# Kernel tuning notes

Hardware: AMD Instinct MI355X
Metric: run time of the kernel (lower is better)

## Reference

```python
import jax, jax.numpy as jnp
import numpy as np

N_NODES = 100000
N_EDGES = 1600000
D = 128
N_GRAPHS = 128
N_LAYERS = 3


def setup_inputs() -> dict:
    key = jax.random.key(0)
    ks = jax.random.split(key, 3 + 4 * N_LAYERS)
    x = jax.random.normal(ks[0], (N_NODES, D), dtype=jnp.float32)
    edge_index = jax.random.randint(ks[1], (2, N_EDGES), 0, N_NODES, dtype=jnp.int64)
    batch = jnp.sort(jax.random.randint(ks[2], (N_NODES,), 0, N_GRAPHS, dtype=jnp.int64))
    inp = {"x": x, "edge_index": edge_index, "batch": batch}
    scale = 1.0 / np.sqrt(D)
    for l in range(N_LAYERS):
        inp[f"W1_{l}"] = jax.random.normal(ks[3 + 4 * l], (D, D), dtype=jnp.float32) * scale
        inp[f"b1_{l}"] = jnp.zeros((D,), dtype=jnp.float32)
        inp[f"W2_{l}"] = jax.random.normal(ks[4 + 4 * l], (D, D), dtype=jnp.float32) * scale
        inp[f"b2_{l}"] = jnp.zeros((D,), dtype=jnp.float32)
    return inp


def _gin_conv(x, edge_index, W1, b1, W2, b2):
    # GINConv with eps=0: out = MLP(x + sum_{j in N(i)} x_j)
    msgs = x[edge_index[0]]                                   # [E, D] gather
    agg = jax.ops.segment_sum(msgs, edge_index[1], num_segments=N_NODES)
    h = x + agg
    h = jax.nn.relu(h @ W1 + b1)
    return h @ W2 + b2


def reference(x, edge_index, batch,
              W1_0, b1_0, W2_0, b2_0,
              W1_1, b1_1, W2_1, b2_1,
              W1_2, b1_2, W2_2, b2_2):
    params = [(W1_0, b1_0, W2_0, b2_0), (W1_1, b1_1, W2_1, b2_1), (W1_2, b1_2, W2_2, b2_2)]
    h = x
    for l in range(N_LAYERS - 1):
        h = _gin_conv(h, edge_index, *params[l])
        h = jax.nn.relu(h)  # act; dropout with drop_ratio=0 is identity
    node_emb = _gin_conv(h, edge_index, *params[-1])  # JK='last'
    # global_mean_pool
    sums = jax.ops.segment_sum(node_emb, batch, num_segments=N_GRAPHS)
    counts = jax.ops.segment_sum(jnp.ones((N_NODES, 1), node_emb.dtype), batch, num_segments=N_GRAPHS)
    graph_emb = sums / jnp.maximum(counts, 1.0)
    return graph_emb
```

## Files before the change

kernel.cpp:

```cpp
#include <hip/hip_runtime.h>
#include <hip/hip_bf16.h>

#define N_NODES 100000
#define N_PAD   100032
#define N_EDGES 1600000
#define DIM 128
#define N_GRAPHS 128
#define NBKT 98
#define BSTRIDE 18432
#define GRID_FUSED 3126
#define POOL_BLKS ((N_NODES + 127) / 128)
#define B1_BATCH 4096
#define B1_GRID ((N_EDGES + B1_BATCH - 1) / B1_BATCH)
#define XPREP_BLKS 12500
#define WPREP_BLKS 384
#define SUMS_BLKS 64

typedef unsigned short u16;
typedef unsigned int u32;
typedef __attribute__((ext_vector_type(8))) short bf16x8;
typedef __attribute__((ext_vector_type(8))) unsigned short u16x8;
typedef __attribute__((ext_vector_type(4))) float f32x4;

#define MFMA(A, B, C) __builtin_amdgcn_mfma_f32_16x16x32_bf16(A, B, C, 0, 0, 0)

__device__ __forceinline__ u16 f2bf(float x) {
    u32 u = __float_as_uint(x);
    u = (u + 0x7FFFu + ((u >> 16) & 1u)) >> 16;
    return (u16)u;
}
__device__ __forceinline__ float bf2f(u16 u) {
    return __uint_as_float(((u32)u) << 16);
}

__global__ __launch_bounds__(256) void bucket1_kernel(const int* __restrict__ src,
                                                      const int* __restrict__ dst,
                                                      u32* __restrict__ cursorB,
                                                      u32* __restrict__ pairs) {
    __shared__ int lh[NBKT];
    __shared__ u32 lbase[NBKT];
    int t = threadIdx.x;
    if (t < NBKT) lh[t] = 0;
    __syncthreads();
    int e0 = blockIdx.x * B1_BATCH;
    int d[16], s[16], rk[16];
#pragma unroll
    for (int k = 0; k < 16; ++k) {
        int e = e0 + t + k * 256;
        if (e < N_EDGES) {
            d[k] = dst[e];
            s[k] = src[e];
            rk[k] = atomicAdd(&lh[d[k] >> 10], 1);
        }
    }
    __syncthreads();
    if (t < NBKT) lbase[t] = atomicAdd(&cursorB[t], (u32)lh[t]) + (u32)(t * BSTRIDE);
    __syncthreads();
#pragma unroll
    for (int k = 0; k < 16; ++k) {
        int e = e0 + t + k * 256;
        if (e < N_EDGES) {
            u32 pos = lbase[d[k] >> 10] + (u32)rk[k];
            pairs[pos] = ((u32)(d[k] & 1023) << 22) | (u32)s[k];
        }
    }
}

__global__ __launch_bounds__(1024) void bucket2_kernel(const u32* __restrict__ cursorB,
                                                       const u32* __restrict__ pairs,
                                                       int* __restrict__ row_ptr,
                                                       int* __restrict__ csr) {
    __shared__ int lh[1024];
    __shared__ int rc[1024];
    __shared__ int bs[128];
    int b = blockIdx.x, t = threadIdx.x;

    if (t < 128) bs[t] = (t < NBKT) ? (int)cursorB[t] : 0;
    __syncthreads();
    for (int off = 1; off < 128; off <<= 1) {
        int v = (t < 128 && t >= off) ? bs[t - off] : 0;
        __syncthreads();
        if (t < 128) bs[t] += v;
        __syncthreads();
    }
    int cnt = (int)cursorB[b];
    int bbase = (b == 0) ? 0 : bs[b - 1];

    lh[t] = 0;
    __syncthreads();
    const u32* pb = pairs + (size_t)b * BSTRIDE;
    for (int i = t; i < cnt; i += 1024) atomicAdd(&lh[__builtin_nontemporal_load(pb + i) >> 22], 1);
    __syncthreads();

    int own = lh[t];
    for (int off = 1; off < 1024; off <<= 1) {
        int v = (t >= off) ? lh[t - off] : 0;
        __syncthreads();
        lh[t] += v;
        __syncthreads();
    }
    int excl = lh[t] - own;
    int node = b * 1024 + t;
    if (node < N_NODES) row_ptr[node] = bbase + excl;
    if (b == 0 && t == 0) row_ptr[N_NODES] = N_EDGES;
    rc[t] = bbase + excl;
    __syncthreads();

    for (int i = t; i < cnt; i += 1024) {
        u32 p = __builtin_nontemporal_load(pb + i);
        int pos = atomicAdd(&rc[p >> 22], 1);
        csr[pos] = (int)(p & 0x3FFFFFu);
    }
}

struct WPrepArgs {
    const float* w[6];
    u16* buf[6];
};
__global__ __launch_bounds__(256) void prep_kernel(const float* __restrict__ x,
                                                   u16* __restrict__ hb,
                                                   WPrepArgs p,
                                                   float* __restrict__ sums) {
    int b = blockIdx.x, t = threadIdx.x;
    if (b < XPREP_BLKS) {
        int i = b * 256 + t;
        if (i < N_NODES * 32) {
            float4 v = ((const float4*)x)[i];
            ushort4 o;
            o.x = f2bf(v.x); o.y = f2bf(v.y); o.z = f2bf(v.z); o.w = f2bf(v.w);
            ((ushort4*)hb)[i] = o;
        }
    } else if (b < XPREP_BLKS + WPREP_BLKS) {
        int bb = b - XPREP_BLKS;
        int m = bb >> 6;
        int idx = (bb & 63) * 256 + t;
        int n = idx >> 7, k = idx & 127;
        float v = p.w[m][k * 128 + n];
        u16 hi = f2bf(v);
        p.buf[m][idx] = hi;
        p.buf[m][idx + 16384] = f2bf(v - bf2f(hi));
    } else {
        int i = (b - XPREP_BLKS - WPREP_BLKS) * 256 + t;
        if (i < N_GRAPHS * DIM) sums[i] = 0.f;
    }
}

#define HS 136
__global__ __launch_bounds__(256, 4) void gin_layer(const u16* __restrict__ hin,
                                                    const int* __restrict__ rp,
                                                    const int* __restrict__ csr,
                                                    const u16* __restrict__ W1,
                                                    const float* __restrict__ b1,
                                                    const u16* __restrict__ W2,
                                                    const float* __restrict__ b2,
                                                    u16* __restrict__ hout, int relu) {
    __shared__ u16 Hh[32 * HS];
    __shared__ u16 Hl[32 * HS];
    int tid = threadIdx.x;
    int lane = tid & 63, wave = tid >> 6;
    int m16 = lane & 15, quad = lane >> 4;
    int colBase = wave * 32;
    int r0 = blockIdx.x * 32;

    {
        int qw = tid >> 4;
        int f  = tid & 15;
        const u16x8* h8 = (const u16x8*)hin;
#pragma unroll
        for (int j = 0; j < 2; ++j) {
            int nl = qw * 2 + j;
            int n = r0 + nl;
            float a[8];
            if (n < N_NODES) {
                u16x8 sv = h8[(size_t)n * 16 + f];
#pragma unroll
                for (int r = 0; r < 8; ++r) a[r] = bf2f(sv[r]);
                int s = rp[n], e = rp[n + 1];
                int i = s;
                for (; i + 8 <= e; i += 8) {
                    u16x8 v0 = h8[(size_t)csr[i + 0] * 16 + f];
                    u16x8 v1 = h8[(size_t)csr[i + 1] * 16 + f];
                    u16x8 v2 = h8[(size_t)csr[i + 2] * 16 + f];
                    u16x8 v3 = h8[(size_t)csr[i + 3] * 16 + f];
                    u16x8 v4 = h8[(size_t)csr[i + 4] * 16 + f];
                    u16x8 v5 = h8[(size_t)csr[i + 5] * 16 + f];
                    u16x8 v6 = h8[(size_t)csr[i + 6] * 16 + f];
                    u16x8 v7 = h8[(size_t)csr[i + 7] * 16 + f];
#pragma unroll
                    for (int r = 0; r < 8; ++r)
                        a[r] += ((bf2f(v0[r]) + bf2f(v1[r])) + (bf2f(v2[r]) + bf2f(v3[r]))) +
                                ((bf2f(v4[r]) + bf2f(v5[r])) + (bf2f(v6[r]) + bf2f(v7[r])));
                }
                for (; i < e; ++i) {
                    u16x8 v = h8[(size_t)csr[i] * 16 + f];
#pragma unroll
                    for (int r = 0; r < 8; ++r) a[r] += bf2f(v[r]);
                }
            } else {
#pragma unroll
                for (int r = 0; r < 8; ++r) a[r] = 0.f;
            }
            u16x8 o;
#pragma unroll
            for (int r = 0; r < 8; ++r) o[r] = f2bf(a[r]);
            *(u16x8*)&Hh[nl * HS + f * 8] = o;
        }
    }
    __syncthreads();

    bf16x8 aH[2][4];
#pragma unroll
    for (int p = 0; p < 2; ++p)
#pragma unroll
        for (int kb = 0; kb < 4; ++kb)
            aH[p][kb] = *(const bf16x8*)&Hh[(p * 16 + m16) * HS + kb * 32 + quad * 8];
    __syncthreads();

    float b1v[2][4], b2v[2][4];
#pragma unroll
    for (int nt = 0; nt < 2; ++nt)
#pragma unroll
        for (int rg = 0; rg < 4; ++rg) {
            int col = colBase + nt * 16 + quad * 4 + rg;
            b1v[nt][rg] = b1[col];
            b2v[nt][rg] = b2[col];
        }

    f32x4 z = {0.f, 0.f, 0.f, 0.f};

    bf16x8 W1H[2][4], W1L[2][4];
#pragma unroll
    for (int nt = 0; nt < 2; ++nt) {
        int n = colBase + nt * 16 + m16;
#pragma unroll
        for (int kb = 0; kb < 4; ++kb) {
            int off = n * 128 + kb * 32 + quad * 8;
            W1H[nt][kb] = *(const bf16x8*)(W1 + off);
            W1L[nt][kb] = *(const bf16x8*)(W1 + off + 16384);
        }
    }

    f32x4 acc[2][2];
#pragma unroll
    for (int p = 0; p < 2; ++p) { acc[p][0] = z; acc[p][1] = z; }

#pragma unroll
    for (int kb = 0; kb < 4; ++kb) {
#pragma unroll
        for (int p = 0; p < 2; ++p) {
            acc[p][0] = MFMA(W1H[0][kb], aH[p][kb], acc[p][0]);
            acc[p][1] = MFMA(W1H[1][kb], aH[p][kb], acc[p][1]);
            acc[p][0] = MFMA(W1L[0][kb], aH[p][kb], acc[p][0]);
            acc[p][1] = MFMA(W1L[1][kb], aH[p][kb], acc[p][1]);
        }
    }

#pragma unroll
    for (int p = 0; p < 2; ++p) {
#pragma unroll
        for (int nt = 0; nt < 2; ++nt) {
            ushort4 hv, lv;
#pragma unroll
            for (int rg = 0; rg < 4; ++rg) {
                float v = fmaxf(acc[p][nt][rg] + b1v[nt][rg], 0.f);
                u16 hi = f2bf(v);
                ((u16*)&hv)[rg] = hi;
                ((u16*)&lv)[rg] = f2bf(v - bf2f(hi));
            }
            int off = (p * 16 + m16) * HS + colBase + nt * 16 + quad * 4;
            *(ushort4*)&Hh[off] = hv;
            *(ushort4*)&Hl[off] = lv;
        }
    }
    __syncthreads();

    bf16x8 W2H[2][4], W2L[2][4];
#pragma unroll
    for (int nt = 0; nt < 2; ++nt) {
        int n = colBase + nt * 16 + m16;
#pragma unroll
        for (int kb = 0; kb < 4; ++kb) {
            int off = n * 128 + kb * 32 + quad * 8;
            W2H[nt][kb] = *(const bf16x8*)(W2 + off);
            W2L[nt][kb] = *(const bf16x8*)(W2 + off + 16384);
        }
    }

    f32x4 acc2[2][2];
#pragma unroll
    for (int p = 0; p < 2; ++p) { acc2[p][0] = z; acc2[p][1] = z; }
#pragma unroll
    for (int kb = 0; kb < 4; ++kb) {
#pragma unroll
        for (int p = 0; p < 2; ++p) {
            int off = (p * 16 + m16) * HS + kb * 32 + quad * 8;
            bf16x8 hH = *(const bf16x8*)(&Hh[off]);
            bf16x8 hL = *(const bf16x8*)(&Hl[off]);
            acc2[p][0] = MFMA(W2H[0][kb], hH, acc2[p][0]);
            acc2[p][1] = MFMA(W2H[1][kb], hH, acc2[p][1]);
            acc2[p][0] = MFMA(W2H[0][kb], hL, acc2[p][0]);
            acc2[p][1] = MFMA(W2H[1][kb], hL, acc2[p][1]);
            acc2[p][0] = MFMA(W2L[0][kb], hH, acc2[p][0]);
            acc2[p][1] = MFMA(W2L[1][kb], hH, acc2[p][1]);
        }
    }

#pragma unroll
    for (int p = 0; p < 2; ++p) {
        size_t row = (size_t)r0 + p * 16 + m16;
#pragma unroll
        for (int nt = 0; nt < 2; ++nt) {
            int col = colBase + nt * 16 + quad * 4;
            ushort4 o;
#pragma unroll
            for (int rg = 0; rg < 4; ++rg) {
                float v = acc2[p][nt][rg] + b2v[nt][rg];
                if (relu) v = fmaxf(v, 0.f);
                ((u16*)&o)[rg] = f2bf(v);
            }
            *(ushort4*)(hout + row * 128 + col) = o;
        }
    }
}

__global__ __launch_bounds__(256) void psum_kernel(const u16* __restrict__ h,
                                                   const int* __restrict__ batch,
                                                   float* __restrict__ sums) {
    __shared__ int sBatch[128];
    int blk = blockIdx.x, t = threadIdx.x;
    int n0 = blk * 128;
    int nEnd = min(n0 + 128, N_NODES);
    if (t < 128 && n0 + t < N_NODES) sBatch[t] = batch[n0 + t];
    __syncthreads();

    int j = t & 127;
    int half = t >> 7;
    int s = n0 + half * 64;
    int e = min(s + 64, nEnd);

    float acc = 0.f;
    int cur = -1;
    for (int n = s; n < e; ++n) {
        int g = sBatch[n - n0];
        if (g != cur) {
            if (cur >= 0) atomicAdd(&sums[cur * 128 + j], acc);
            cur = g;
            acc = 0.f;
        }
        acc += bf2f(h[(size_t)n * 128 + j]);
    }
    if (cur >= 0) atomicAdd(&sums[cur * 128 + j], acc);
}

__global__ __launch_bounds__(128) void pdiv_kernel(const float* __restrict__ sums,
                                                   const int* __restrict__ batch,
                                                   float* __restrict__ out) {
    __shared__ int sB[2];
    int g = blockIdx.x;
    if (threadIdx.x < 2) {
        int target = g + threadIdx.x;
        int lo = 0, hi = N_NODES;
        while (lo < hi) {
            int m = (lo + hi) >> 1;
            if (batch[m] < target) lo = m + 1; else hi = m;
        }
        sB[threadIdx.x] = lo;
    }
    __syncthreads();
    float cnt = (float)(sB[1] - sB[0]);
    out[g * 128 + threadIdx.x] = sums[g * 128 + threadIdx.x] / fmaxf(cnt, 1.f);
}

extern "C" void kernel_launch(void* const* d_in, const int* in_sizes, int n_in,
                              void* d_out, int out_size, void* d_ws, size_t ws_size,
                              hipStream_t stream) {
    const float* x     = (const float*)d_in[0];
    const int*   ei    = (const int*)d_in[1];
    const int*   batch = (const int*)d_in[2];
    const int*   eSrc  = ei;
    const int*   eDst  = ei + N_EDGES;

    const float* W1[3] = {(const float*)d_in[3], (const float*)d_in[7],  (const float*)d_in[11]};
    const float* b1[3] = {(const float*)d_in[4], (const float*)d_in[8],  (const float*)d_in[12]};
    const float* W2[3] = {(const float*)d_in[5], (const float*)d_in[9],  (const float*)d_in[13]};
    const float* b2[3] = {(const float*)d_in[6], (const float*)d_in[10], (const float*)d_in[14]};

    float* P2 = (float*)d_ws;
    u16*   planeB = (u16*)P2;
    u16*   planeA = (u16*)(P2 + (size_t)N_PAD * DIM);
    u16*   Ah = planeA + (size_t)N_PAD * DIM;
    u16*   Wb = Ah + (size_t)N_PAD * DIM;
    int*   row_ptr = (int*)(Wb + 6 * 32768);
    u32*   cursorB = (u32*)(row_ptr + N_NODES + 8);
    int*   csr     = (int*)(cursorB + 128);
    float* sums    = (float*)(csr + N_EDGES);
    u32*   pairs   = (u32*)P2;

    hipMemsetAsync(cursorB, 0, 128 * sizeof(u32), stream);
    bucket1_kernel<<<B1_GRID, 256, 0, stream>>>(eSrc, eDst, cursorB, pairs);
    bucket2_kernel<<<NBKT, 1024, 0, stream>>>(cursorB, pairs, row_ptr, csr);

    WPrepArgs wp;
    for (int l = 0; l < 3; ++l) {
        wp.w[2 * l]       = W1[l];
        wp.w[2 * l + 1]   = W2[l];
        wp.buf[2 * l]     = Wb + (size_t)(2 * l) * 32768;
        wp.buf[2 * l + 1] = Wb + (size_t)(2 * l + 1) * 32768;
    }
    prep_kernel<<<XPREP_BLKS + WPREP_BLKS + SUMS_BLKS, 256, 0, stream>>>(x, planeA, wp, sums);

    u16* hin  = planeA;
    u16* hout = planeB;
    for (int l = 0; l < 3; ++l) {
        gin_layer<<<GRID_FUSED, 256, 0, stream>>>(hin, row_ptr, csr,
                                                  Wb + (size_t)(2 * l) * 32768, b1[l],
                                                  Wb + (size_t)(2 * l + 1) * 32768, b2[l],
                                                  hout, (l < 2) ? 1 : 0);
        u16* tmp = hin; hin = hout; hout = tmp;
    }
    psum_kernel<<<POOL_BLKS, 256, 0, stream>>>(hin, batch, sums);
    pdiv_kernel<<<N_GRAPHS, 128, 0, stream>>>(sums, batch, (float*)d_out);
}
```

Before: 512.9 us.

## Warp-specialize GIN layer into persistent gather producer and MFMA consumer

Splits each 512-thread block into two halves. 256 threads gather and sum neighbour features into a double-buffered LDS tile of 64 rows. The other 256 threads run the two bf16 split-precision MLP matmuls on the previous tile. The grid becomes a persistent 512-block launch that loops over row groups, with tile size doubled from 32 to 64 rows. The goal is to overlap the latency-bound gather with MFMA compute. In exchange, fewer threads are issuing gather loads concurrently, more LDS is used per block, and occupancy is lower.

```diff
diff --git a/kernel.cpp b/kernel.cpp
--- a/kernel.cpp
+++ b/kernel.cpp
@@ -8,7 +8,8 @@
 #define N_GRAPHS 128
 #define NBKT 98
 #define BSTRIDE 18432
-#define GRID_FUSED 3126
+#define NGRP 1563
+#define GRID_PC 512
 #define POOL_BLKS ((N_NODES + 127) / 128)
 #define B1_BATCH 4096
 #define B1_GRID ((N_EDGES + B1_BATCH - 1) / B1_BATCH)
@@ -146,7 +147,57 @@
 }
 
 #define HS 136
-__global__ __launch_bounds__(256, 4) void gin_layer(const u16* __restrict__ hin,
+
+__device__ __forceinline__ void gather_half(const u16* __restrict__ hin,
+                                            const int* __restrict__ rp,
+                                            const int* __restrict__ csr,
+                                            u16* __restrict__ Gbuf,
+                                            int r0, int tid, int jbase) {
+    int qw = tid >> 4;
+    int f  = tid & 15;
+    const u16x8* h8 = (const u16x8*)hin;
+#pragma unroll
+    for (int j = jbase; j < jbase + 2; ++j) {
+        int nl = qw * 4 + j;
+        int n = r0 + nl;
+        float a[8];
+        if (n < N_NODES) {
+            u16x8 sv = h8[(size_t)n * 16 + f];
+#pragma unroll
+            for (int r = 0; r < 8; ++r) a[r] = bf2f(sv[r]);
+            int s = rp[n], e = rp[n + 1];
+            int i = s;
+            for (; i + 8 <= e; i += 8) {
+                u16x8 v0 = h8[(size_t)csr[i + 0] * 16 + f];
+                u16x8 v1 = h8[(size_t)csr[i + 1] * 16 + f];
+                u16x8 v2 = h8[(size_t)csr[i + 2] * 16 + f];
+                u16x8 v3 = h8[(size_t)csr[i + 3] * 16 + f];
+                u16x8 v4 = h8[(size_t)csr[i + 4] * 16 + f];
+                u16x8 v5 = h8[(size_t)csr[i + 5] * 16 + f];
+                u16x8 v6 = h8[(size_t)csr[i + 6] * 16 + f];
+                u16x8 v7 = h8[(size_t)csr[i + 7] * 16 + f];
+#pragma unroll
+                for (int r = 0; r < 8; ++r)
+                    a[r] += ((bf2f(v0[r]) + bf2f(v1[r])) + (bf2f(v2[r]) + bf2f(v3[r]))) +
+                            ((bf2f(v4[r]) + bf2f(v5[r])) + (bf2f(v6[r]) + bf2f(v7[r])));
+            }
+            for (; i < e; ++i) {
+                u16x8 v = h8[(size_t)csr[i] * 16 + f];
+#pragma unroll
+                for (int r = 0; r < 8; ++r) a[r] += bf2f(v[r]);
+            }
+        } else {
+#pragma unroll
+            for (int r = 0; r < 8; ++r) a[r] = 0.f;
+        }
+        u16x8 o;
+#pragma unroll
+        for (int r = 0; r < 8; ++r) o[r] = f2bf(a[r]);
+        *(u16x8*)&Gbuf[nl * HS + f * 8] = o;
+    }
+}
+
+__global__ __launch_bounds__(512, 2) void gin_layer(const u16* __restrict__ hin,
                                                     const int* __restrict__ rp,
                                                     const int* __restrict__ csr,
                                                     const u16* __restrict__ W1,
@@ -154,171 +205,155 @@
                                                     const u16* __restrict__ W2,
                                                     const float* __restrict__ b2,
                                                     u16* __restrict__ hout, int relu) {
-    __shared__ u16 Hh[32 * HS];
-    __shared__ u16 Hl[32 * HS];
+    __shared__ u16 G[2][64 * HS];
+    __shared__ u16 Hh[64 * HS];
+    __shared__ u16 Hl[64 * HS];
     int tid = threadIdx.x;
-    int lane = tid & 63, wave = tid >> 6;
-    int m16 = lane & 15, quad = lane >> 4;
-    int colBase = wave * 32;
-    int r0 = blockIdx.x * 32;
-
-    {
-        int qw = tid >> 4;
-        int f  = tid & 15;
-        const u16x8* h8 = (const u16x8*)hin;
-#pragma unroll
-        for (int j = 0; j < 2; ++j) {
-            int nl = qw * 2 + j;
-            int n = r0 + nl;
-            float a[8];
-            if (n < N_NODES) {
-                u16x8 sv = h8[(size_t)n * 16 + f];
-#pragma unroll
-                for (int r = 0; r < 8; ++r) a[r] = bf2f(sv[r]);
-                int s = rp[n], e = rp[n + 1];
-                int i = s;
-                for (; i + 8 <= e; i += 8) {
-                    u16x8 v0 = h8[(size_t)csr[i + 0] * 16 + f];
-                    u16x8 v1 = h8[(size_t)csr[i + 1] * 16 + f];
-                    u16x8 v2 = h8[(size_t)csr[i + 2] * 16 + f];
-                    u16x8 v3 = h8[(size_t)csr[i + 3] * 16 + f];
-                    u16x8 v4 = h8[(size_t)csr[i + 4] * 16 + f];
-                    u16x8 v5 = h8[(size_t)csr[i + 5] * 16 + f];
-                    u16x8 v6 = h8[(size_t)csr[i + 6] * 16 + f];
-                    u16x8 v7 = h8[(size_t)csr[i + 7] * 16 + f];
-#pragma unroll
-                    for (int r = 0; r < 8; ++r)
-                        a[r] += ((bf2f(v0[r]) + bf2f(v1[r])) + (bf2f(v2[r]) + bf2f(v3[r]))) +
-                                ((bf2f(v4[r]) + bf2f(v5[r])) + (bf2f(v6[r]) + bf2f(v7[r])));
-                }
-                for (; i < e; ++i) {
-                    u16x8 v = h8[(size_t)csr[i] * 16 + f];
-#pragma unroll
-                    for (int r = 0; r < 8; ++r) a[r] += bf2f(v[r]);
-                }
+    int b = blockIdx.x;
+
+    int K = 0;
+    for (int g = b; g < NGRP; g += GRID_PC) ++K;
+
+    if (tid < 256) {
+        gather_half(hin, rp, csr, G[0], b * 64, tid, 0);
+        gather_half(hin, rp, csr, G[0], b * 64, tid, 2);
+        __syncthreads();
+        for (int k = 0; k < K; ++k) {
+            int gn = b + (k + 1) * GRID_PC;
+            if (gn < NGRP) {
+                u16* Gn = G[(k + 1) & 1];
+                gather_half(hin, rp, csr, Gn, gn * 64, tid, 0);
+                __syncthreads();
+                gather_half(hin, rp, csr, Gn, gn * 64, tid, 2);
+                __syncthreads();
             } else {
-#pragma unroll
-                for (int r = 0; r < 8; ++r) a[r] = 0.f;
-            }
-            u16x8 o;
-#pragma unroll
-            for (int r = 0; r < 8; ++r) o[r] = f2bf(a[r]);
-            *(u16x8*)&Hh[nl * HS + f * 8] = o;
-        }
-    }
-    __syncthreads();
-
-    bf16x8 aH[2][4];
-#pragma unroll
-    for (int p = 0; p < 2; ++p)
-#pragma unroll
-        for (int kb = 0; kb < 4; ++kb)
-            aH[p][kb] = *(const bf16x8*)&Hh[(p * 16 + m16) * HS + kb * 32 + quad * 8];
-    __syncthreads();
-
-    float b1v[2][4], b2v[2][4];
-#pragma unroll
-    for (int nt = 0; nt < 2; ++nt)
-#pragma unroll
-        for (int rg = 0; rg < 4; ++rg) {
-            int col = colBase + nt * 16 + quad * 4 + rg;
-            b1v[nt][rg] = b1[col];
-            b2v[nt][rg] = b2[col];
-        }
-
-    f32x4 z = {0.f, 0.f, 0.f, 0.f};
-
-    bf16x8 W1H[2][4], W1L[2][4];
-#pragma unroll
-    for (int nt = 0; nt < 2; ++nt) {
-        int n = colBase + nt * 16 + m16;
-#pragma unroll
-        for (int kb = 0; kb < 4; ++kb) {
-            int off = n * 128 + kb * 32 + quad * 8;
-            W1H[nt][kb] = *(const bf16x8*)(W1 + off);
-            W1L[nt][kb] = *(const bf16x8*)(W1 + off + 16384);
-        }
-    }
-
-    f32x4 acc[2][2];
-#pragma unroll
-    for (int p = 0; p < 2; ++p) { acc[p][0] = z; acc[p][1] = z; }
-
-#pragma unroll
-    for (int kb = 0; kb < 4; ++kb) {
-#pragma unroll
-        for (int p = 0; p < 2; ++p) {
-            acc[p][0] = MFMA(W1H[0][kb], aH[p][kb], acc[p][0]);
-            acc[p][1] = MFMA(W1H[1][kb], aH[p][kb], acc[p][1]);
-            acc[p][0] = MFMA(W1L[0][kb], aH[p][kb], acc[p][0]);
-            acc[p][1] = MFMA(W1L[1][kb], aH[p][kb], acc[p][1]);
-        }
-    }
-
-#pragma unroll
-    for (int p = 0; p < 2; ++p) {
-#pragma unroll
-        for (int nt = 0; nt < 2; ++nt) {
-            ushort4 hv, lv;
+                __syncthreads();
+                __syncthreads();
+            }
+        }
+    } else {
+        int tc = tid - 256;
+        int lane = tc & 63, wave = tc >> 6;
+        int m16 = lane & 15, quad = lane >> 4;
+        int colBase = wave * 32;
+
+        float b1v[2][4], b2v[2][4];
+#pragma unroll
+        for (int nt = 0; nt < 2; ++nt)
 #pragma unroll
             for (int rg = 0; rg < 4; ++rg) {
-                float v = fmaxf(acc[p][nt][rg] + b1v[nt][rg], 0.f);
-                u16 hi = f2bf(v);
-                ((u16*)&hv)[rg] = hi;
-                ((u16*)&lv)[rg] = f2bf(v - bf2f(hi));
-            }
-            int off = (p * 16 + m16) * HS + colBase + nt * 16 + quad * 4;
-            *(ushort4*)&Hh[off] = hv;
-            *(ushort4*)&Hl[off] = lv;
-        }
-    }
-    __syncthreads();
-
-    bf16x8 W2H[2][4], W2L[2][4];
-#pragma unroll
-    for (int nt = 0; nt < 2; ++nt) {
-        int n = colBase + nt * 16 + m16;
-#pragma unroll
-        for (int kb = 0; kb < 4; ++kb) {
-            int off = n * 128 + kb * 32 + quad * 8;
-            W2H[nt][kb] = *(const bf16x8*)(W2 + off);
-            W2L[nt][kb] = *(const bf16x8*)(W2 + off + 16384);
-        }
-    }
-
-    f32x4 acc2[2][2];
-#pragma unroll
-    for (int p = 0; p < 2; ++p) { acc2[p][0] = z; acc2[p][1] = z; }
-#pragma unroll
-    for (int kb = 0; kb < 4; ++kb) {
-#pragma unroll
-        for (int p = 0; p < 2; ++p) {
-            int off = (p * 16 + m16) * HS + kb * 32 + quad * 8;
-            bf16x8 hH = *(const bf16x8*)(&Hh[off]);
-            bf16x8 hL = *(const bf16x8*)(&Hl[off]);
-            acc2[p][0] = MFMA(W2H[0][kb], hH, acc2[p][0]);
-            acc2[p][1] = MFMA(W2H[1][kb], hH, acc2[p][1]);
-            acc2[p][0] = MFMA(W2H[0][kb], hL, acc2[p][0]);
-            acc2[p][1] = MFMA(W2H[1][kb], hL, acc2[p][1]);
-            acc2[p][0] = MFMA(W2L[0][kb], hH, acc2[p][0]);
-            acc2[p][1] = MFMA(W2L[1][kb], hH, acc2[p][1]);
-        }
-    }
-
-#pragma unroll
-    for (int p = 0; p < 2; ++p) {
-        size_t row = (size_t)r0 + p * 16 + m16;
-#pragma unroll
-        for (int nt = 0; nt < 2; ++nt) {
-            int col = colBase + nt * 16 + quad * 4;
-            ushort4 o;
-#pragma unroll
-            for (int rg = 0; rg < 4; ++rg) {
-                float v = acc2[p][nt][rg] + b2v[nt][rg];
-                if (relu) v = fmaxf(v, 0.f);
-                ((u16*)&o)[rg] = f2bf(v);
-            }
-            *(ushort4*)(hout + row * 128 + col) = o;
+                int col = colBase + nt * 16 + quad * 4 + rg;
+                b1v[nt][rg] = b1[col];
+                b2v[nt][rg] = b2[col];
+            }
+        f32x4 z = {0.f, 0.f, 0.f, 0.f};
+
+        __syncthreads();
+        for (int k = 0; k < K; ++k) {
+            int g = b + k * GRID_PC;
+            const u16* Gc = G[k & 1];
+
+            bf16x8 aH[4][4];
+#pragma unroll
+            for (int p = 0; p < 4; ++p)
+#pragma unroll
+                for (int kb = 0; kb < 4; ++kb)
+                    aH[p][kb] = *(const bf16x8*)&Gc[(p * 16 + m16) * HS + kb * 32 + quad * 8];
+
+            bf16x8 W1H[2][4], W1L[2][4];
+#pragma unroll
+            for (int nt = 0; nt < 2; ++nt) {
+                int n = colBase + nt * 16 + m16;
+#pragma unroll
+                for (int kb = 0; kb < 4; ++kb) {
+                    int off = n * 128 + kb * 32 + quad * 8;
+                    W1H[nt][kb] = *(const bf16x8*)(W1 + off);
+                    W1L[nt][kb] = *(const bf16x8*)(W1 + off + 16384);
+                }
+            }
+
+            f32x4 acc[4][2];
+#pragma unroll
+            for (int p = 0; p < 4; ++p) { acc[p][0] = z; acc[p][1] = z; }
+#pragma unroll
+            for (int kb = 0; kb < 4; ++kb) {
+#pragma unroll
+                for (int p = 0; p < 4; ++p) {
+                    acc[p][0] = MFMA(W1H[0][kb], aH[p][kb], acc[p][0]);
+                    acc[p][1] = MFMA(W1H[1][kb], aH[p][kb], acc[p][1]);
+                    acc[p][0] = MFMA(W1L[0][kb], aH[p][kb], acc[p][0]);
+                    acc[p][1] = MFMA(W1L[1][kb], aH[p][kb], acc[p][1]);
+                }
+            }
+
+#pragma unroll
+            for (int p = 0; p < 4; ++p) {
+#pragma unroll
+                for (int nt = 0; nt < 2; ++nt) {
+                    ushort4 hv, lv;
+#pragma unroll
+                    for (int rg = 0; rg < 4; ++rg) {
+                        float v = fmaxf(acc[p][nt][rg] + b1v[nt][rg], 0.f);
+                        u16 hi = f2bf(v);
+                        ((u16*)&hv)[rg] = hi;
+                        ((u16*)&lv)[rg] = f2bf(v - bf2f(hi));
+                    }
+                    int off = (p * 16 + m16) * HS + colBase + nt * 16 + quad * 4;
+                    *(ushort4*)&Hh[off] = hv;
+                    *(ushort4*)&Hl[off] = lv;
+                }
+            }
+            __syncthreads();
+
+            bf16x8 W2H[2][4], W2L[2][4];
+#pragma unroll
+            for (int nt = 0; nt < 2; ++nt) {
+                int n = colBase + nt * 16 + m16;
+#pragma unroll
+                for (int kb = 0; kb < 4; ++kb) {
+                    int off = n * 128 + kb * 32 + quad * 8;
+                    W2H[nt][kb] = *(const bf16x8*)(W2 + off);
+                    W2L[nt][kb] = *(const bf16x8*)(W2 + off + 16384);
+                }
+            }
+
+            f32x4 acc2[4][2];
+#pragma unroll
+            for (int p = 0; p < 4; ++p) { acc2[p][0] = z; acc2[p][1] = z; }
+#pragma unroll
+            for (int kb = 0; kb < 4; ++kb) {
+#pragma unroll
+                for (int p = 0; p < 4; ++p) {
+                    int off = (p * 16 + m16) * HS + kb * 32 + quad * 8;
+                    bf16x8 hH = *(const bf16x8*)(&Hh[off]);
+                    bf16x8 hL = *(const bf16x8*)(&Hl[off]);
+                    acc2[p][0] = MFMA(W2H[0][kb], hH, acc2[p][0]);
+                    acc2[p][1] = MFMA(W2H[1][kb], hH, acc2[p][1]);
+                    acc2[p][0] = MFMA(W2H[0][kb], hL, acc2[p][0]);
+                    acc2[p][1] = MFMA(W2H[1][kb], hL, acc2[p][1]);
+                    acc2[p][0] = MFMA(W2L[0][kb], hH, acc2[p][0]);
+                    acc2[p][1] = MFMA(W2L[1][kb], hH, acc2[p][1]);
+                }
+            }
+            __syncthreads();
+
+            int r0 = g * 64;
+#pragma unroll
+            for (int p = 0; p < 4; ++p) {
+                size_t row = (size_t)r0 + p * 16 + m16;
+#pragma unroll
+                for (int nt = 0; nt < 2; ++nt) {
+                    int col = colBase + nt * 16 + quad * 4;
+                    ushort4 o;
+#pragma unroll
+                    for (int rg = 0; rg < 4; ++rg) {
+                        float v = acc2[p][nt][rg] + b2v[nt][rg];
+                        if (relu) v = fmaxf(v, 0.f);
+                        ((u16*)&o)[rg] = f2bf(v);
+                    }
+                    *(ushort4*)(hout + row * 128 + col) = o;
+                }
+            }
         }
     }
 }
@@ -412,10 +447,10 @@
     u16* hin  = planeA;
     u16* hout = planeB;
     for (int l = 0; l < 3; ++l) {
-        gin_layer<<<GRID_FUSED, 256, 0, stream>>>(hin, row_ptr, csr,
-                                                  Wb + (size_t)(2 * l) * 32768, b1[l],
-                                                  Wb + (size_t)(2 * l + 1) * 32768, b2[l],
-                                                  hout, (l < 2) ? 1 : 0);
+        gin_layer<<<GRID_PC, 512, 0, stream>>>(hin, row_ptr, csr,
+                                               Wb + (size_t)(2 * l) * 32768, b1[l],
+                                               Wb + (size_t)(2 * l + 1) * 32768, b2[l],
+                                               hout, (l < 2) ? 1 : 0);
         u16* tmp = hin; hin = hout; hout = tmp;
     }
     psum_kernel<<<POOL_BLKS, 256, 0, stream>>>(hin, batch, sums);
```

Measured after the change: 743.5 us. 45.0% more time.

## Give each wave its own 16-row tile to remove block-wide barriers

Applied to the files above, without the earlier changes.

The fused GIN layer now assigns one 16-node tile per wave instead of one 32-node tile per block shared across four waves. Each wave gathers its own rows, with 16 features per lane, into private LDS and computes all 128 output columns itself. This removes every __syncthreads and halves the grid. The cost is that each wave reloads the full W1/W2 hi/lo matrices from global memory (or cache) per 16 rows, and the neighbor unroll drops from 8 to 4.

```diff
diff --git a/kernel.cpp b/kernel.cpp
--- a/kernel.cpp
+++ b/kernel.cpp
@@ -8,7 +8,8 @@
 #define N_GRAPHS 128
 #define NBKT 98
 #define BSTRIDE 18432
-#define GRID_FUSED 3126
+#define TILES (N_PAD / 16)
+#define GRID_FUSED 1563
 #define POOL_BLKS ((N_NODES + 127) / 128)
 #define B1_BATCH 4096
 #define B1_GRID ((N_EDGES + B1_BATCH - 1) / B1_BATCH)
@@ -154,172 +155,138 @@
                                                     const u16* __restrict__ W2,
                                                     const float* __restrict__ b2,
                                                     u16* __restrict__ hout, int relu) {
-    __shared__ u16 Hh[32 * HS];
-    __shared__ u16 Hl[32 * HS];
+    __shared__ u16 lds[4][2][16 * HS];
     int tid = threadIdx.x;
-    int lane = tid & 63, wave = tid >> 6;
+    int wave = tid >> 6, lane = tid & 63;
+    u16* A  = &lds[wave][0][0];
+    u16* Hh = &lds[wave][1][0];
+
+    int tile = blockIdx.x * 4 + wave;
+    int r0 = tile * 16;
+
+    int rh = lane >> 3;
+    int fl = lane & 7;
+    const u16x8* h8 = (const u16x8*)hin;
+#pragma unroll
+    for (int h = 0; h < 2; ++h) {
+        int n = r0 + h * 8 + rh;
+        float a[16];
+        if (n < N_NODES) {
+            u16x8 s0 = h8[(size_t)n * 16 + 2 * fl];
+            u16x8 s1 = h8[(size_t)n * 16 + 2 * fl + 1];
+#pragma unroll
+            for (int r = 0; r < 8; ++r) { a[r] = bf2f(s0[r]); a[8 + r] = bf2f(s1[r]); }
+            int s = rp[n], e = rp[n + 1];
+            int i = s;
+            for (; i + 4 <= e; i += 4) {
+                int j0 = csr[i], j1 = csr[i + 1], j2 = csr[i + 2], j3 = csr[i + 3];
+                u16x8 v00 = h8[(size_t)j0 * 16 + 2 * fl], v01 = h8[(size_t)j0 * 16 + 2 * fl + 1];
+                u16x8 v10 = h8[(size_t)j1 * 16 + 2 * fl], v11 = h8[(size_t)j1 * 16 + 2 * fl + 1];
+                u16x8 v20 = h8[(size_t)j2 * 16 + 2 * fl], v21 = h8[(size_t)j2 * 16 + 2 * fl + 1];
+                u16x8 v30 = h8[(size_t)j3 * 16 + 2 * fl], v31 = h8[(size_t)j3 * 16 + 2 * fl + 1];
+#pragma unroll
+                for (int r = 0; r < 8; ++r) {
+                    a[r]     += (bf2f(v00[r]) + bf2f(v10[r])) + (bf2f(v20[r]) + bf2f(v30[r]));
+                    a[8 + r] += (bf2f(v01[r]) + bf2f(v11[r])) + (bf2f(v21[r]) + bf2f(v31[r]));
+                }
+            }
+            for (; i < e; ++i) {
+                int j = csr[i];
+                u16x8 v0 = h8[(size_t)j * 16 + 2 * fl], v1 = h8[(size_t)j * 16 + 2 * fl + 1];
+#pragma unroll
+                for (int r = 0; r < 8; ++r) { a[r] += bf2f(v0[r]); a[8 + r] += bf2f(v1[r]); }
+            }
+        } else {
+#pragma unroll
+            for (int r = 0; r < 16; ++r) a[r] = 0.f;
+        }
+        u16x8 o0, o1;
+#pragma unroll
+        for (int r = 0; r < 8; ++r) { o0[r] = f2bf(a[r]); o1[r] = f2bf(a[8 + r]); }
+        *(u16x8*)&A[(h * 8 + rh) * HS + fl * 16] = o0;
+        *(u16x8*)&A[(h * 8 + rh) * HS + fl * 16 + 8] = o1;
+    }
+
     int m16 = lane & 15, quad = lane >> 4;
-    int colBase = wave * 32;
-    int r0 = blockIdx.x * 32;
-
-    {
-        int qw = tid >> 4;
-        int f  = tid & 15;
-        const u16x8* h8 = (const u16x8*)hin;
-#pragma unroll
-        for (int j = 0; j < 2; ++j) {
-            int nl = qw * 2 + j;
-            int n = r0 + nl;
-            float a[8];
-            if (n < N_NODES) {
-                u16x8 sv = h8[(size_t)n * 16 + f];
-#pragma unroll
-                for (int r = 0; r < 8; ++r) a[r] = bf2f(sv[r]);
-                int s = rp[n], e = rp[n + 1];
-                int i = s;
-                for (; i + 8 <= e; i += 8) {
-                    u16x8 v0 = h8[(size_t)csr[i + 0] * 16 + f];
-                    u16x8 v1 = h8[(size_t)csr[i + 1] * 16 + f];
-                    u16x8 v2 = h8[(size_t)csr[i + 2] * 16 + f];
-                    u16x8 v3 = h8[(size_t)csr[i + 3] * 16 + f];
-                    u16x8 v4 = h8[(size_t)csr[i + 4] * 16 + f];
-                    u16x8 v5 = h8[(size_t)csr[i + 5] * 16 + f];
-                    u16x8 v6 = h8[(size_t)csr[i + 6] * 16 + f];
-                    u16x8 v7 = h8[(size_t)csr[i + 7] * 16 + f];
-#pragma unroll
-                    for (int r = 0; r < 8; ++r)
-                        a[r] += ((bf2f(v0[r]) + bf2f(v1[r])) + (bf2f(v2[r]) + bf2f(v3[r]))) +
-                                ((bf2f(v4[r]) + bf2f(v5[r])) + (bf2f(v6[r]) + bf2f(v7[r])));
-                }
-                for (; i < e; ++i) {
-                    u16x8 v = h8[(size_t)csr[i] * 16 + f];
-#pragma unroll
-                    for (int r = 0; r < 8; ++r) a[r] += bf2f(v[r]);
-                }
-            } else {
-#pragma unroll
-                for (int r = 0; r < 8; ++r) a[r] = 0.f;
-            }
-            u16x8 o;
-#pragma unroll
-            for (int r = 0; r < 8; ++r) o[r] = f2bf(a[r]);
-            *(u16x8*)&Hh[nl * HS + f * 8] = o;
-        }
-    }
-    __syncthreads();
-
-    bf16x8 aH[2][4];
-#pragma unroll
-    for (int p = 0; p < 2; ++p)
-#pragma unroll
-        for (int kb = 0; kb < 4; ++kb)
-            aH[p][kb] = *(const bf16x8*)&Hh[(p * 16 + m16) * HS + kb * 32 + quad * 8];
-    __syncthreads();
-
-    float b1v[2][4], b2v[2][4];
-#pragma unroll
-    for (int nt = 0; nt < 2; ++nt)
+    f32x4 z = {0.f, 0.f, 0.f, 0.f};
+
+    bf16x8 aH[4];
+#pragma unroll
+    for (int kb = 0; kb < 4; ++kb)
+        aH[kb] = *(const bf16x8*)&A[m16 * HS + kb * 32 + quad * 8];
+
+    f32x4 acc[8];
+#pragma unroll
+    for (int nt = 0; nt < 8; ++nt) {
+        int ncol = nt * 16 + m16;
+        bf16x8 WH[4], WL[4];
+#pragma unroll
+        for (int kb = 0; kb < 4; ++kb) {
+            int off = ncol * 128 + kb * 32 + quad * 8;
+            WH[kb] = *(const bf16x8*)(W1 + off);
+            WL[kb] = *(const bf16x8*)(W1 + off + 16384);
+        }
+        acc[nt] = z;
+#pragma unroll
+        for (int kb = 0; kb < 4; ++kb) {
+            acc[nt] = MFMA(WH[kb], aH[kb], acc[nt]);
+            acc[nt] = MFMA(WL[kb], aH[kb], acc[nt]);
+        }
+    }
+
+#pragma unroll
+    for (int nt = 0; nt < 8; ++nt) {
+        ushort4 hv, lv;
 #pragma unroll
         for (int rg = 0; rg < 4; ++rg) {
-            int col = colBase + nt * 16 + quad * 4 + rg;
-            b1v[nt][rg] = b1[col];
-            b2v[nt][rg] = b2[col];
-        }
-
-    f32x4 z = {0.f, 0.f, 0.f, 0.f};
-
-    bf16x8 W1H[2][4], W1L[2][4];
-#pragma unroll
-    for (int nt = 0; nt < 2; ++nt) {
-        int n = colBase + nt * 16 + m16;
+            float v = fmaxf(acc[nt][rg] + b1[nt * 16 + quad * 4 + rg], 0.f);
+            u16 hi = f2bf(v);
+            ((u16*)&hv)[rg] = hi;
+            ((u16*)&lv)[rg] = f2bf(v - bf2f(hi));
+        }
+        int off = m16 * HS + nt * 16 + quad * 4;
+        *(ushort4*)&Hh[off] = hv;
+        *(ushort4*)&A[off]  = lv;
+    }
+
+    bf16x8 hH[4], hL[4];
+#pragma unroll
+    for (int kb = 0; kb < 4; ++kb) {
+        hH[kb] = *(const bf16x8*)&Hh[m16 * HS + kb * 32 + quad * 8];
+        hL[kb] = *(const bf16x8*)&A[m16 * HS + kb * 32 + quad * 8];
+    }
+    f32x4 acc2[8];
+#pragma unroll
+    for (int nt = 0; nt < 8; ++nt) {
+        int ncol = nt * 16 + m16;
+        bf16x8 WH[4], WL[4];
 #pragma unroll
         for (int kb = 0; kb < 4; ++kb) {
-            int off = n * 128 + kb * 32 + quad * 8;
-            W1H[nt][kb] = *(const bf16x8*)(W1 + off);
-            W1L[nt][kb] = *(const bf16x8*)(W1 + off + 16384);
-        }
-    }
-
-    f32x4 acc[2][2];
-#pragma unroll
-    for (int p = 0; p < 2; ++p) { acc[p][0] = z; acc[p][1] = z; }
-
-#pragma unroll
-    for (int kb = 0; kb < 4; ++kb) {
-#pragma unroll
-        for (int p = 0; p < 2; ++p) {
-            acc[p][0] = MFMA(W1H[0][kb], aH[p][kb], acc[p][0]);
-            acc[p][1] = MFMA(W1H[1][kb], aH[p][kb], acc[p][1]);
-            acc[p][0] = MFMA(W1L[0][kb], aH[p][kb], acc[p][0]);
-            acc[p][1] = MFMA(W1L[1][kb], aH[p][kb], acc[p][1]);
-        }
-    }
-
-#pragma unroll
-    for (int p = 0; p < 2; ++p) {
-#pragma unroll
-        for (int nt = 0; nt < 2; ++nt) {
-            ushort4 hv, lv;
-#pragma unroll
-            for (int rg = 0; rg < 4; ++rg) {
-                float v = fmaxf(acc[p][nt][rg] + b1v[nt][rg], 0.f);
-                u16 hi = f2bf(v);
-                ((u16*)&hv)[rg] = hi;
-                ((u16*)&lv)[rg] = f2bf(v - bf2f(hi));
-            }
-            int off = (p * 16 + m16) * HS + colBase + nt * 16 + quad * 4;
-            *(ushort4*)&Hh[off] = hv;
-            *(ushort4*)&Hl[off] = lv;
-        }
-    }
-    __syncthreads();
-
-    bf16x8 W2H[2][4], W2L[2][4];
-#pragma unroll
-    for (int nt = 0; nt < 2; ++nt) {
-        int n = colBase + nt * 16 + m16;
+            int off = ncol * 128 + kb * 32 + quad * 8;
+            WH[kb] = *(const bf16x8*)(W2 + off);
+            WL[kb] = *(const bf16x8*)(W2 + off + 16384);
+        }
+        acc2[nt] = z;
 #pragma unroll
         for (int kb = 0; kb < 4; ++kb) {
-            int off = n * 128 + kb * 32 + quad * 8;
-            W2H[nt][kb] = *(const bf16x8*)(W2 + off);
-            W2L[nt][kb] = *(const bf16x8*)(W2 + off + 16384);
-        }
-    }
-
-    f32x4 acc2[2][2];
-#pragma unroll
-    for (int p = 0; p < 2; ++p) { acc2[p][0] = z; acc2[p][1] = z; }
-#pragma unroll
-    for (int kb = 0; kb < 4; ++kb) {
-#pragma unroll
-        for (int p = 0; p < 2; ++p) {
-            int off = (p * 16 + m16) * HS + kb * 32 + quad * 8;
-            bf16x8 hH = *(const bf16x8*)(&Hh[off]);
-            bf16x8 hL = *(const bf16x8*)(&Hl[off]);
-            acc2[p][0] = MFMA(W2H[0][kb], hH, acc2[p][0]);
-            acc2[p][1] = MFMA(W2H[1][kb], hH, acc2[p][1]);
-            acc2[p][0] = MFMA(W2H[0][kb], hL, acc2[p][0]);
-            acc2[p][1] = MFMA(W2H[1][kb], hL, acc2[p][1]);
-            acc2[p][0] = MFMA(W2L[0][kb], hH, acc2[p][0]);
-            acc2[p][1] = MFMA(W2L[1][kb], hH, acc2[p][1]);
-        }
-    }
-
-#pragma unroll
-    for (int p = 0; p < 2; ++p) {
-        size_t row = (size_t)r0 + p * 16 + m16;
-#pragma unroll
-        for (int nt = 0; nt < 2; ++nt) {
-            int col = colBase + nt * 16 + quad * 4;
-            ushort4 o;
-#pragma unroll
-            for (int rg = 0; rg < 4; ++rg) {
-                float v = acc2[p][nt][rg] + b2v[nt][rg];
-                if (relu) v = fmaxf(v, 0.f);
-                ((u16*)&o)[rg] = f2bf(v);
-            }
-            *(ushort4*)(hout + row * 128 + col) = o;
-        }
+            acc2[nt] = MFMA(WH[kb], hH[kb], acc2[nt]);
+            acc2[nt] = MFMA(WH[kb], hL[kb], acc2[nt]);
+            acc2[nt] = MFMA(WL[kb], hH[kb], acc2[nt]);
+        }
+    }
+
+    size_t row = (size_t)r0 + m16;
+#pragma unroll
+    for (int nt = 0; nt < 8; ++nt) {
+        int col = nt * 16 + quad * 4;
+        ushort4 o;
+#pragma unroll
+        for (int rg = 0; rg < 4; ++rg) {
+            float v = acc2[nt][rg] + b2[col + rg];
+            if (relu) v = fmaxf(v, 0.f);
+            ((u16*)&o)[rg] = f2bf(v);
+        }
+        *(ushort4*)(hout + row * 128 + col) = o;
     }
 }
 
```

After: 655.2 us. 1.28x slower.
